# Kernel optimization log

Hardware: AMD Instinct MI355X
Metric: run time of the kernel (lower is better)

The kernel has to match this reference:

```python
import jax, jax.numpy as jnp
import numpy as np

B, N, D_IN, D_PROJ, C = 1024, 50000, 768, 128, 100
BW2 = float(D_PROJ)   # RBF bandwidth^2
EPS = 1e-10


def setup_inputs() -> dict:
    key = jax.random.key(0)
    ks = jax.random.split(key, 6)
    x = jax.random.normal(ks[0], (B, D_IN), jnp.float32)
    X = jax.random.normal(ks[1], (N, D_IN), jnp.float32)
    # learned projection (Linear D_IN -> D_PROJ); scale keeps projected coords ~N(0,1)
    Wp = jax.random.normal(ks[2], (D_IN, D_PROJ), jnp.float32) * (D_IN ** -0.5)
    bp = jnp.zeros((D_PROJ,), jnp.float32)
    Y = jax.random.randint(ks[3], (N,), 0, C, jnp.int32)
    SorP_train = jax.random.normal(ks[4], (N, C), jnp.float32)
    SorP_q = jax.random.normal(ks[5], (B, C), jnp.float32)
    return dict(x=x, X=X, Wp=Wp, bp=bp, Y=Y, SorP_train=SorP_train, SorP_q=SorP_q)


def _perm_locs(SorP):
    # locs = argsort(argsort(SorP, descending)) per row
    sort_idx = jnp.argsort(-SorP, axis=-1)
    return jnp.argsort(sort_idx, axis=-1)


def reference(x, X, Wp, bp, Y, SorP_train, SorP_q):
    px = x @ Wp + bp            # [B, D_PROJ]
    pX = X @ Wp + bp            # [N, D_PROJ]
    # squared euclidean distances via GEMM
    sqd = ((px * px).sum(-1, keepdims=True)
           + (pX * pX).sum(-1)[None, :]
           - 2.0 * (px @ pX.T))                     # [B, N]
    Kis = jnp.exp(-sqd / (2.0 * BW2))               # RBF kernel, self-sim == 1
    # drop_self: zero out (near-)self matches
    Kis = jnp.where(Kis < 1.0 - EPS, Kis, 0.0)
    # rows with ~zero total mass -> uniform eps
    Kis = jnp.where(Kis.sum(1, keepdims=True) > EPS, Kis, EPS)
    # MODE_SORT label encoding: one_hot(locs_train[i, Y[i]])
    locs_t = _perm_locs(SorP_train)                 # [N, C]
    Y1h = jax.nn.one_hot(locs_t[jnp.arange(N), Y], C, dtype=jnp.float32)
    pred = Kis @ Y1h                                # [B, C]
    pred = pred / pred.sum(1, keepdims=True)
    # per-sample reorder (vectorized gather instead of the python loop)
    locs_q = _perm_locs(SorP_q)                     # [B, C]
    return jnp.take_along_axis(pred, locs_q, axis=1)
```

## Files before the change

kernel.cpp:

```cpp
#include <hip/hip_runtime.h>


typedef short  bf8v  __attribute__((ext_vector_type(8)));
typedef float  f32x4 __attribute__((ext_vector_type(4)));

#define NTRAIN 50000
#define NPAD   50048
#define NTILES 391
#define BQ     1024
#define DIN    768
#define DP     128
#define NCLS   100
#define PSTRIDE 102
#define PCOLS  104
#define FIXS   2097152.0f
#define FIXI   (1.0f / 2097152.0f)
#define NBX    (NPAD / 64)
#define NBQ    (BQ / 64)
#define NBL    ((NPAD + 3) / 4)

__device__ __forceinline__ short f2bf(float x) {
    unsigned u = __float_as_uint(x);
    u += 0x7FFFu + ((u >> 16) & 1u);
    return (short)(u >> 16);
}

#define AS1U(p) ((const __attribute__((address_space(1))) unsigned int*)(unsigned long long)(p))
#define AS3U(p) ((__attribute__((address_space(3))) unsigned int*)(unsigned int)(unsigned long long)(p))

__global__ __launch_bounds__(256) void k_pack_wp(const float* __restrict__ Wp,
                                                 short* __restrict__ WpP) {
    int tid = blockIdx.x * 256 + threadIdx.x;
    if (tid >= 24 * 8 * 64) return;
    int l = tid & 63, cb = (tid >> 6) & 7, q = tid >> 9;
    int c = cb * 16 + (l & 15);
    int g = l >> 4;
    bf8v o;
#pragma unroll
    for (int j = 0; j < 8; ++j) {
        int k = q * 32 + g * 8 + j;
        o[j] = f2bf(Wp[k * DP + c]);
    }
    *reinterpret_cast<bf8v*>(WpP + (size_t)tid * 8) = o;
}

__device__ __forceinline__ void proj_body(const float* __restrict__ Xin,
                                          const short* __restrict__ WpP,
                                          const float* __restrict__ bp,
                                          short* __restrict__ outP,
                                          float* __restrict__ normv,
                                          int Mreal, int blk,
                                          float* __restrict__ Xlds) {
    const int tid = threadIdx.x;
    const int w = tid >> 6, l = tid & 63, g = l >> 4, li = l & 15;
    const int rowblk = blk * 64;

    f32x4 acc[8];
#pragma unroll
    for (int cb = 0; cb < 8; ++cb) acc[cb] = (f32x4){0.f, 0.f, 0.f, 0.f};

#define STAGE64(lbuf, kb)                                                     \
    {                                                                         \
        _Pragma("unroll")                                                     \
        for (int it = 0; it < 4; ++it) {                                      \
            int s  = w * 256 + it * 64 + l;                                   \
            int r  = s >> 4;                                                  \
            int c4 = (s & 15) ^ (r & 7);                                      \
            int rg = rowblk + r;                                              \
            rg = (rg < Mreal) ? rg : (Mreal - 1);                             \
            const float* gp = Xin + (size_t)rg * DIN + (kb) * 64 + c4 * 4;    \
            const float* lp = (lbuf) + (w * 256 + it * 64) * 4;               \
            __builtin_amdgcn_global_load_lds(AS1U(gp), AS3U(lp), 16, 0, 0);   \
        }                                                                     \
    }
#define ISSUE_B(dst, kb)                                                      \
    {                                                                         \
        _Pragma("unroll")                                                     \
        for (int f = 0; f < 16; ++f)                                          \
            dst[f] = *reinterpret_cast<const bf8v*>(                          \
                WpP + ((size_t)((kb) * 16 + f) * 64 + l) * 8);                \
    }

    bf8v breg[16];
    float4 a[4];

    STAGE64(Xlds, 0);
    STAGE64(Xlds + 4096, 1);
    ISSUE_B(breg, 0);

#pragma unroll 1
    for (int kb = 0; kb < 12; ++kb) {
        float* tb = Xlds + (kb & 1) * 4096;
        asm volatile("s_waitcnt vmcnt(20)" ::: "memory");
        {
            const float* rbase = tb + (w * 16 + li) * 64;
#pragma unroll
            for (int kc = 0; kc < 2; ++kc) {
                int s0 = (kc * 8 + g * 2)     ^ (li & 7);
                int s1 = (kc * 8 + g * 2 + 1) ^ (li & 7);
                a[kc * 2]     = *reinterpret_cast<const float4*>(rbase + s0 * 4);
                a[kc * 2 + 1] = *reinterpret_cast<const float4*>(rbase + s1 * 4);
            }
        }
        asm volatile("s_waitcnt lgkmcnt(0)" ::: "memory");
        __builtin_amdgcn_sched_barrier(0);
        if (kb + 2 < 12) {
            STAGE64(tb, kb + 2);
            asm volatile("s_waitcnt vmcnt(4)" ::: "memory");
        } else {
            asm volatile("s_waitcnt vmcnt(0)" ::: "memory");
        }
        __builtin_amdgcn_sched_barrier(0);
#pragma unroll
        for (int kc = 0; kc < 2; ++kc) {
            float4 a0 = a[kc * 2], a1 = a[kc * 2 + 1];
            bf8v af;
            af[0] = f2bf(a0.x); af[1] = f2bf(a0.y);
            af[2] = f2bf(a0.z); af[3] = f2bf(a0.w);
            af[4] = f2bf(a1.x); af[5] = f2bf(a1.y);
            af[6] = f2bf(a1.z); af[7] = f2bf(a1.w);
#pragma unroll
            for (int cb = 0; cb < 8; ++cb)
                acc[cb] = __builtin_amdgcn_mfma_f32_16x16x32_bf16(
                              af, breg[kc * 8 + cb], acc[cb], 0, 0, 0);
        }
        if (kb + 1 < 12) ISSUE_B(breg, kb + 1);
    }
#undef STAGE64
#undef ISSUE_B

    float bpv[8];
#pragma unroll
    for (int cb = 0; cb < 8; ++cb) bpv[cb] = bp[cb * 16 + li];
#pragma unroll
    for (int cb = 0; cb < 8; ++cb)
#pragma unroll
        for (int r = 0; r < 4; ++r) acc[cb][r] += bpv[cb];

#pragma unroll
    for (int r = 0; r < 4; ++r) {
        float s = 0.f;
#pragma unroll
        for (int cb = 0; cb < 8; ++cb) {
            float v = acc[cb][r];
            s += v * v;
        }
        s += __shfl_xor(s, 1);
        s += __shfl_xor(s, 2);
        s += __shfl_xor(s, 4);
        s += __shfl_xor(s, 8);
        int grow = rowblk + w * 16 + 4 * g + r;
        if (li == 0) normv[grow] = (grow < Mreal) ? s : 1e30f;
    }

#pragma unroll
    for (int cb = 0; cb < 8; ++cb) {
        int d = cb * 16 + li;
        int q = d >> 5, g2 = (d & 31) >> 3, j = d & 7;
#pragma unroll
        for (int r = 0; r < 4; ++r) {
            int grow = rowblk + w * 16 + 4 * g + r;
            float v = (grow < Mreal) ? acc[cb][r] : 0.f;
            size_t e = ((size_t)((grow >> 4) * 4 + q) * 64 +
                        (g2 * 16 + (grow & 15))) * 8 + j;
            outP[e] = f2bf(v);
        }
    }
}

__global__ __launch_bounds__(256, 3) void k_front(const float* __restrict__ X,
                                                  const float* __restrict__ x,
                                                  const short* __restrict__ WpP,
                                                  const float* __restrict__ bp,
                                                  short* __restrict__ pXp,
                                                  short* __restrict__ pxq,
                                                  float* __restrict__ kn,
                                                  float* __restrict__ qn,
                                                  const float* __restrict__ S,
                                                  const int* __restrict__ Y,
                                                  int* __restrict__ lab) {
    __shared__ __align__(16) float Xlds[2 * 64 * 64];
    int b = blockIdx.x;
    if (b < NBX) {
        proj_body(X, WpP, bp, pXp, kn, NTRAIN, b, Xlds);
        return;
    }
    if (b < NBX + NBQ) {
        proj_body(x, WpP, bp, pxq, qn, BQ, b - NBX, Xlds);
        return;
    }
    int w = threadIdx.x >> 6, l = threadIdx.x & 63;
    int i = (b - NBX - NBQ) * 4 + w;
    if (i >= NPAD) return;
    int cnt = 0;
    if (i < NTRAIN) {
        int y = Y[i];
        float t = S[(size_t)i * NCLS + y];
        float v1 = S[(size_t)i * NCLS + l];
        bool p1 = (v1 > t) || (v1 == t && l < y);
        unsigned long long b1 = __ballot(p1);
        bool p2 = false;
        if (l < NCLS - 64) {
            float v2 = S[(size_t)i * NCLS + 64 + l];
            p2 = (v2 > t) || (v2 == t && (64 + l) < y);
        }
        unsigned long long b2 = __ballot(p2);
        cnt = __popcll(b1) + __popcll(b2);
    }
    if (l == 0) lab[i] = cnt;
}

__global__ __launch_bounds__(256) void k_main(const short* __restrict__ pxp,
                                              const short* __restrict__ pXp,
                                              const float* __restrict__ qn,
                                              const float* __restrict__ kn,
                                              const int* __restrict__ lab,
                                              float* __restrict__ part,
                                              int NCH) {
    __shared__ __align__(16) unsigned plds[128 * PSTRIDE];
    const int tid = threadIdx.x;
    const int w = tid >> 6, l = tid & 63, g = l >> 4, li = l & 15;
    const int ch = blockIdx.x;
    const int bt = blockIdx.y;

    for (int s = tid; s < 128 * PSTRIDE; s += 256) plds[s] = 0u;
    __syncthreads();

    bf8v af[2][4];
#pragma unroll
    for (int rb = 0; rb < 2; ++rb)
#pragma unroll
        for (int q = 0; q < 4; ++q) {
            int RB = bt * 8 + w * 2 + rb;
            af[rb][q] = *reinterpret_cast<const bf8v*>(
                            pxp + (size_t)((RB * 4 + q) * 64 + l) * 8);
        }
    float qnv[2][4];
#pragma unroll
    for (int rb = 0; rb < 2; ++rb)
#pragma unroll
        for (int r = 0; r < 4; ++r)
            qnv[rb][r] = qn[bt * 128 + w * 32 + rb * 16 + 4 * g + r];

#pragma unroll 1
    for (int t = ch; t < NTILES; t += NCH) {
        const int i0 = t * 128;
        const int RB0 = i0 >> 4;
        float knv8[8];
        int   labv8[8];
#pragma unroll
        for (int ib = 0; ib < 8; ++ib) {
            knv8[ib]  = kn[i0 + ib * 16 + li];
            labv8[ib] = lab[i0 + ib * 16 + li];
        }
        bf8v bfr[4][4];
#pragma unroll
        for (int p = 0; p < 3; ++p)
#pragma unroll
            for (int q = 0; q < 4; ++q)
                bfr[p][q] = *reinterpret_cast<const bf8v*>(
                    pXp + (size_t)(((RB0 + p) * 4 + q) * 64 + l) * 8);
#pragma unroll
        for (int ib = 0; ib < 8; ++ib) {
            if (ib + 3 < 8) {
#pragma unroll
                for (int q = 0; q < 4; ++q)
                    bfr[(ib + 3) & 3][q] = *reinterpret_cast<const bf8v*>(
                        pXp + (size_t)(((RB0 + ib + 3) * 4 + q) * 64 + l) * 8);
            }
            f32x4 s0 = (f32x4){0.f, 0.f, 0.f, 0.f};
            f32x4 s1 = (f32x4){0.f, 0.f, 0.f, 0.f};
#pragma unroll
            for (int q = 0; q < 4; ++q) {
                s0 = __builtin_amdgcn_mfma_f32_16x16x32_bf16(af[0][q], bfr[ib & 3][q], s0, 0, 0, 0);
                s1 = __builtin_amdgcn_mfma_f32_16x16x32_bf16(af[1][q], bfr[ib & 3][q], s1, 0, 0, 0);
            }
            const float knv  = knv8[ib];
            const int   labv = labv8[ib];
#pragma unroll
            for (int rb = 0; rb < 2; ++rb) {
                f32x4 sv = rb ? s1 : s0;
#pragma unroll
                for (int r = 0; r < 4; ++r) {
                    float sqd = qnv[rb][r] + knv - 2.f * sv[r];
                    float kis = __expf(sqd * (-1.f / 256.f));
                    kis = (kis < 1.0f) ? kis : 0.f;
                    unsigned qv = (unsigned)__float2uint_rn(kis * FIXS);
                    int rowl = w * 32 + rb * 16 + 4 * g + r;
                    atomicAdd(&plds[rowl * PSTRIDE + labv], qv);
                }
            }
        }
    }

#pragma unroll 1
    for (int rr = 0; rr < 32; ++rr) {
        int row = w * 32 + rr;
        if (l < PSTRIDE / 2) {
            uint2 u = *reinterpret_cast<const uint2*>(&plds[row * PSTRIDE + l * 2]);
            float2 v = make_float2((float)u.x * FIXI, (float)u.y * FIXI);
            int grow = bt * 128 + row;
            *reinterpret_cast<float2*>(
                &part[((size_t)grow * NCH + ch) * PCOLS + l * 2]) = v;
        }
    }
}

__global__ __launch_bounds__(256) void k_final(const float* __restrict__ part,
                                               const float* __restrict__ SorPq,
                                               float* __restrict__ out,
                                               int NCH) {
    __shared__ float sp[NCLS];
    __shared__ float pr2[2][PCOLS];
    int t = threadIdx.x, b = blockIdx.x;
    int c = t & 127, h = t >> 7;
    if (h == 1 && c < NCLS) sp[c] = SorPq[(size_t)b * NCLS + c];
    if (c < NCLS) {
        float s = 0.f;
        int half = NCH >> 1;
        const float* p = part + ((size_t)b * NCH + (size_t)h * half) * PCOLS + c;
        for (int ch = 0; ch < half; ++ch) s += p[(size_t)ch * PCOLS];
        pr2[h][c] = s;
    }
    __syncthreads();
    if (t < NCLS) pr2[0][t] += pr2[1][t];
    __syncthreads();
    if (t < NCLS) {
        float tot = 0.f;
        for (int k = 0; k < NCLS; ++k) tot += pr2[0][k];
        float s = sp[t];
        int r = 0;
        for (int k = 0; k < NCLS; ++k) {
            float sk = sp[k];
            r += (sk > s || (sk == s && k < t)) ? 1 : 0;
        }
        out[(size_t)b * NCLS + t] = pr2[0][r] / tot;
    }
}

extern "C" void kernel_launch(void* const* d_in, const int* in_sizes, int n_in,
                              void* d_out, int out_size, void* d_ws, size_t ws_size,
                              hipStream_t stream) {
    const float* x    = (const float*)d_in[0];
    const float* X    = (const float*)d_in[1];
    const float* Wp   = (const float*)d_in[2];
    const float* bp   = (const float*)d_in[3];
    const int*   Y    = (const int*)  d_in[4];
    const float* SPt  = (const float*)d_in[5];
    const float* SPq  = (const float*)d_in[6];
    float* out = (float*)d_out;

    char* ws = (char*)d_ws;
    short* WpP = (short*)(ws + 0);
    short* pXp = (short*)(ws + 196608);
    short* pxq = (short*)(ws + 13008896);
    float* kn  = (float*)(ws + 13271040);
    float* qn  = (float*)(ws + 13471232);
    int*   lab = (int*)  (ws + 13475328);
    float* part= (float*)(ws + 13675520);

    const size_t base = 13675520;
    const size_t per  = (size_t)BQ * PCOLS * 4;
    int NCH = 96;
    if (ws_size > base) {
        size_t fit = (ws_size - base) / per;
        if ((size_t)NCH > fit) NCH = (int)fit;
    } else {
        NCH = 8;
    }
    NCH &= ~7;
    if (NCH < 8) NCH = 8;

    k_pack_wp<<<48, 256, 0, stream>>>(Wp, WpP);
    k_front<<<NBX + NBQ + NBL, 256, 0, stream>>>(X, x, WpP, bp, pXp, pxq,
                                                 kn, qn, SPt, Y, lab);
    k_main<<<dim3(NCH, 8), 256, 0, stream>>>(pxq, pXp, qn, kn, lab, part, NCH);
    k_final<<<BQ, 256, 0, stream>>>(part, SPq, out, NCH);
}
```

Measured before the change: 111.9 us.

## Use atomic work-stealing tile scheduler in main kernel and integer partial sums

```diff
diff --git a/kernel.cpp b/kernel.cpp
--- a/kernel.cpp
+++ b/kernel.cpp
@@ -17,7 +17,7 @@
 #define FIXI   (1.0f / 2097152.0f)
 #define NBX    (NPAD / 64)
 #define NBQ    (BQ / 64)
-#define NBL    ((NPAD + 3) / 4)
+#define NBL    ((NPAD + 15) / 16)
 
 __device__ __forceinline__ short f2bf(float x) {
     unsigned u = __float_as_uint(x);
@@ -29,7 +29,9 @@
 #define AS3U(p) ((__attribute__((address_space(3))) unsigned int*)(unsigned int)(unsigned long long)(p))
 
 __global__ __launch_bounds__(256) void k_pack_wp(const float* __restrict__ Wp,
-                                                 short* __restrict__ WpP) {
+                                                 short* __restrict__ WpP,
+                                                 unsigned* __restrict__ cnt) {
+    if (blockIdx.x == 0 && threadIdx.x < 8) cnt[threadIdx.x] = 0u;
     int tid = blockIdx.x * 256 + threadIdx.x;
     if (tid >= 24 * 8 * 64) return;
     int l = tid & 63, cb = (tid >> 6) & 7, q = tid >> 9;
@@ -190,24 +192,27 @@
         return;
     }
     int w = threadIdx.x >> 6, l = threadIdx.x & 63;
-    int i = (b - NBX - NBQ) * 4 + w;
-    if (i >= NPAD) return;
-    int cnt = 0;
-    if (i < NTRAIN) {
-        int y = Y[i];
-        float t = S[(size_t)i * NCLS + y];
-        float v1 = S[(size_t)i * NCLS + l];
-        bool p1 = (v1 > t) || (v1 == t && l < y);
-        unsigned long long b1 = __ballot(p1);
-        bool p2 = false;
-        if (l < NCLS - 64) {
-            float v2 = S[(size_t)i * NCLS + 64 + l];
-            p2 = (v2 > t) || (v2 == t && (64 + l) < y);
-        }
-        unsigned long long b2 = __ballot(p2);
-        cnt = __popcll(b1) + __popcll(b2);
-    }
-    if (l == 0) lab[i] = cnt;
+#pragma unroll 1
+    for (int r4 = 0; r4 < 4; ++r4) {
+        int i = (b - NBX - NBQ) * 16 + w * 4 + r4;
+        if (i >= NPAD) continue;
+        int cnt = 0;
+        if (i < NTRAIN) {
+            int y = Y[i];
+            float t = S[(size_t)i * NCLS + y];
+            float v1 = S[(size_t)i * NCLS + l];
+            bool p1 = (v1 > t) || (v1 == t && l < y);
+            unsigned long long b1 = __ballot(p1);
+            bool p2 = false;
+            if (l < NCLS - 64) {
+                float v2 = S[(size_t)i * NCLS + 64 + l];
+                p2 = (v2 > t) || (v2 == t && (64 + l) < y);
+            }
+            unsigned long long b2 = __ballot(p2);
+            cnt = __popcll(b1) + __popcll(b2);
+        }
+        if (l == 0) lab[i] = cnt;
+    }
 }
 
 __global__ __launch_bounds__(256) void k_main(const short* __restrict__ pxp,
@@ -215,15 +220,18 @@
                                               const float* __restrict__ qn,
                                               const float* __restrict__ kn,
                                               const int* __restrict__ lab,
-                                              float* __restrict__ part,
+                                              unsigned* __restrict__ part,
+                                              unsigned* __restrict__ cnt,
                                               int NCH) {
     __shared__ __align__(16) unsigned plds[128 * PSTRIDE];
+    __shared__ int tsh[2];
     const int tid = threadIdx.x;
     const int w = tid >> 6, l = tid & 63, g = l >> 4, li = l & 15;
     const int ch = blockIdx.x;
     const int bt = blockIdx.y;
 
     for (int s = tid; s < 128 * PSTRIDE; s += 256) plds[s] = 0u;
+    if (tid == 0) tsh[0] = (int)atomicAdd(&cnt[bt], 1u);
     __syncthreads();
 
     bf8v af[2][4];
@@ -242,8 +250,11 @@
         for (int r = 0; r < 4; ++r)
             qnv[rb][r] = qn[bt * 128 + w * 32 + rb * 16 + 4 * g + r];
 
+    int t = tsh[0];
+    int pp = 1;
 #pragma unroll 1
-    for (int t = ch; t < NTILES; t += NCH) {
+    while (t < NTILES) {
+        if (tid == 0) tsh[pp] = (int)atomicAdd(&cnt[bt], 1u);
         const int i0 = t * 128;
         const int RB0 = i0 >> 4;
         float knv8[8];
@@ -291,6 +302,9 @@
                 }
             }
         }
+        __syncthreads();
+        t = tsh[pp];
+        pp ^= 1;
     }
 
 #pragma unroll 1
@@ -298,27 +312,26 @@
         int row = w * 32 + rr;
         if (l < PSTRIDE / 2) {
             uint2 u = *reinterpret_cast<const uint2*>(&plds[row * PSTRIDE + l * 2]);
-            float2 v = make_float2((float)u.x * FIXI, (float)u.y * FIXI);
             int grow = bt * 128 + row;
-            *reinterpret_cast<float2*>(
-                &part[((size_t)grow * NCH + ch) * PCOLS + l * 2]) = v;
-        }
-    }
-}
-
-__global__ __launch_bounds__(256) void k_final(const float* __restrict__ part,
+            *reinterpret_cast<uint2*>(
+                &part[((size_t)grow * NCH + ch) * PCOLS + l * 2]) = u;
+        }
+    }
+}
+
+__global__ __launch_bounds__(256) void k_final(const unsigned* __restrict__ part,
                                                const float* __restrict__ SorPq,
                                                float* __restrict__ out,
                                                int NCH) {
     __shared__ float sp[NCLS];
-    __shared__ float pr2[2][PCOLS];
+    __shared__ unsigned pr2[2][PCOLS];
     int t = threadIdx.x, b = blockIdx.x;
     int c = t & 127, h = t >> 7;
     if (h == 1 && c < NCLS) sp[c] = SorPq[(size_t)b * NCLS + c];
     if (c < NCLS) {
-        float s = 0.f;
+        unsigned s = 0u;
         int half = NCH >> 1;
-        const float* p = part + ((size_t)b * NCH + (size_t)h * half) * PCOLS + c;
+        const unsigned* p = part + ((size_t)b * NCH + (size_t)h * half) * PCOLS + c;
         for (int ch = 0; ch < half; ++ch) s += p[(size_t)ch * PCOLS];
         pr2[h][c] = s;
     }
@@ -327,14 +340,15 @@
     __syncthreads();
     if (t < NCLS) {
         float tot = 0.f;
-        for (int k = 0; k < NCLS; ++k) tot += pr2[0][k];
+        for (int k = 0; k < NCLS; ++k)
+            tot += (float)pr2[0][k] * FIXI;
         float s = sp[t];
         int r = 0;
         for (int k = 0; k < NCLS; ++k) {
             float sk = sp[k];
             r += (sk > s || (sk == s && k < t)) ? 1 : 0;
         }
-        out[(size_t)b * NCLS + t] = pr2[0][r] / tot;
+        out[(size_t)b * NCLS + t] = ((float)pr2[0][r] * FIXI) / tot;
     }
 }
 
@@ -357,9 +371,10 @@
     float* kn  = (float*)(ws + 13271040);
     float* qn  = (float*)(ws + 13471232);
     int*   lab = (int*)  (ws + 13475328);
-    float* part= (float*)(ws + 13675520);
-
-    const size_t base = 13675520;
+    unsigned* cnt  = (unsigned*)(ws + 13675520);
+    unsigned* part = (unsigned*)(ws + 13675648);
+
+    const size_t base = 13675648;
     const size_t per  = (size_t)BQ * PCOLS * 4;
     int NCH = 96;
     if (ws_size > base) {
@@ -371,9 +386,9 @@
     NCH &= ~7;
     if (NCH < 8) NCH = 8;
 
-    k_pack_wp<<<48, 256, 0, stream>>>(Wp, WpP);
+    k_pack_wp<<<48, 256, 0, stream>>>(Wp, WpP, cnt);
     k_front<<<NBX + NBQ + NBL, 256, 0, stream>>>(X, x, WpP, bp, pXp, pxq,
                                                  kn, qn, SPt, Y, lab);
-    k_main<<<dim3(NCH, 8), 256, 0, stream>>>(pxq, pXp, qn, kn, lab, part, NCH);
+    k_main<<<dim3(NCH, 8), 256, 0, stream>>>(pxq, pXp, qn, kn, lab, part, cnt, NCH);
     k_final<<<BQ, 256, 0, stream>>>(part, SPq, out, NCH);
 }
```

Result: slower. 129.0 us (+15.3%).
